# Performance work log

Measured on AMD Instinct MI355X. Metric: run time of the kernel, lower is better.

The kernel has to match this reference:

```python
import jax, jax.numpy as jnp
import numpy as np

B, T, S, D, H, F = 4, 1024, 1024, 1024, 16, 4096
NEG = jnp.float32(-1e9)


def _ln(x, g, b):
    m = jnp.mean(x, axis=-1, keepdims=True)
    v = jnp.mean((x - m) ** 2, axis=-1, keepdims=True)
    return (x - m) * jax.lax.rsqrt(v + 1e-5) * g + b


def _mha(q, k, v, wq, bq, wk, bk, wv, bv, wo, bo, scale, mask, causal, sbias):
    Bq, Tq, Dq = q.shape
    Sk = k.shape[1]
    dk = Dq // H
    Q = (q @ wq.T + bq).reshape(Bq, Tq, H, dk).transpose(0, 2, 1, 3)  # [B,H,T,dk]
    K = (k @ wk.T + bk).reshape(Bq, Sk, H, dk).transpose(0, 2, 1, 3)  # [B,H,S,dk]
    V = (v @ wv.T + bv).reshape(Bq, Sk, H, dk).transpose(0, 2, 1, 3)
    s = jnp.einsum('bhtd,bhsd->bhts', Q, K) / jnp.sqrt(jnp.float32(dk))
    if sbias is not None:
        s = s + scale * sbias[:, None, None, :]
    if mask is not None:
        s = jnp.where(mask == 0, NEG, s)
    if causal is not None:
        s = jnp.where(causal == 0, NEG, s)
    a = jax.nn.softmax(s, axis=-1)
    o = jnp.einsum('bhts,bhsd->bhtd', a, V).transpose(0, 2, 1, 3).reshape(Bq, Tq, Dq)
    return o @ wo.T + bo


def setup_inputs():
    key = jax.random.key(0)
    ks = jax.random.split(key, 16)
    r = lambda i, shape, s=0.02: jax.random.normal(ks[i], shape, dtype=jnp.float32) * s
    z = lambda *shape: jnp.zeros(shape, jnp.float32)
    o = lambda *shape: jnp.ones(shape, jnp.float32)
    inp = dict(
        x=r(0, (B, T, D), 1.0),
        memory=r(1, (B, S, D), 1.0),
        sentence_bias=r(2, (B, S), 1.0),
        trg_mask=jnp.ones((B, 1, 1, T), jnp.int32),
        trg_causal_mask=jnp.tril(jnp.ones((T, T), jnp.int32))[None, None],
        src_mask=jnp.ones((B, 1, 1, S), jnp.int32),
        sa_wq=r(3, (D, D)), sa_bq=z(D), sa_wk=r(4, (D, D)), sa_bk=z(D),
        sa_wv=r(5, (D, D)), sa_bv=z(D), sa_wo=r(6, (D, D)), sa_bo=z(D),
        sa_scale=jnp.float32(0.1),
        ca_wq=r(7, (D, D)), ca_bq=z(D), ca_wk=r(8, (D, D)), ca_bk=z(D),
        ca_wv=r(9, (D, D)), ca_bv=z(D), ca_wo=r(10, (D, D)), ca_bo=z(D),
        ca_scale=jnp.float32(0.1),
        ln1_g=o(D), ln1_b=z(D), ln2_g=o(D), ln2_b=z(D), ln3_g=o(D), ln3_b=z(D),
        ffn_w1=r(11, (F, D)), ffn_b1=z(F), ffn_w2=r(12, (D, F)), ffn_b2=z(D),
    )
    return inp


def reference(x, memory, trg_mask, trg_causal_mask, src_mask, sentence_bias,
              sa_wq, sa_bq, sa_wk, sa_bk, sa_wv, sa_bv, sa_wo, sa_bo, sa_scale,
              ca_wq, ca_bq, ca_wk, ca_bk, ca_wv, ca_bv, ca_wo, ca_bo, ca_scale,
              ln1_g, ln1_b, ln2_g, ln2_b, ln3_g, ln3_b,
              ffn_w1, ffn_b1, ffn_w2, ffn_b2):
    # Faithful quirk: Q comes from normed x, K/V from raw residual stream.
    x = x + _mha(_ln(x, ln1_g, ln1_b), x, x,
                 sa_wq, sa_bq, sa_wk, sa_bk, sa_wv, sa_bv, sa_wo, sa_bo,
                 sa_scale, trg_mask, trg_causal_mask, None)
    x = x + _mha(_ln(x, ln2_g, ln2_b), memory, memory,
                 ca_wq, ca_bq, ca_wk, ca_bk, ca_wv, ca_bv, ca_wo, ca_bo,
                 ca_scale, src_mask, None, sentence_bias)
    h = _ln(x, ln3_g, ln3_b)
    x = x + (jax.nn.relu(h @ ffn_w1.T + ffn_b1) @ ffn_w2.T + ffn_b2)
    return x
```

## Files before the change

### kernel.cpp

```cpp
#include <hip/hip_runtime.h>
#include <hip/hip_bf16.h>
#include <cmath>
#include <stdint.h>

typedef __hip_bfloat16 bf16;
typedef __attribute__((ext_vector_type(8))) __bf16 bf16x8;
typedef __attribute__((ext_vector_type(8))) unsigned short u16x8;
typedef __attribute__((ext_vector_type(4))) float f32x4;

__device__ __forceinline__ void gld16(const void* g, const void* l)
{
    __builtin_amdgcn_global_load_lds(
        (const __attribute__((address_space(1))) unsigned int*)(unsigned long long)g,
        (__attribute__((address_space(3))) unsigned int*)(unsigned int)(unsigned long long)l,
        16, 0, 0);
}

struct CvtSrcs { const float* p[24]; };

__global__ __launch_bounds__(256) void cvt_all(
    CvtSrcs s, bf16* __restrict__ dst,
    const float* __restrict__ lg, const float* __restrict__ lb,
    bf16* __restrict__ lnout)
{
    const int t = threadIdx.x;
    const int i = (blockIdx.x * 256 + t) * 8;
    const int seg = i >> 20;
    const float* sp = s.p[seg] + (i & 1048575);
    const float4 a = *(const float4*)(sp);
    const float4 b = *(const float4*)(sp + 4);
    const float v[8] = {a.x, a.y, a.z, a.w, b.x, b.y, b.z, b.w};
    bf16 tmp[8];
#pragma unroll
    for (int j = 0; j < 8; ++j) tmp[j] = __float2bfloat16(v[j]);
    *(uint4*)(dst + i) = *(const uint4*)tmp;

    if (seg < 4) {
        float s1 = 0.f, s2 = 0.f;
#pragma unroll
        for (int j = 0; j < 8; ++j) { s1 += v[j]; s2 += v[j] * v[j]; }
#pragma unroll
        for (int off = 32; off > 0; off >>= 1) {
            s1 += __shfl_xor(s1, off, 64);
            s2 += __shfl_xor(s2, off, 64);
        }
        __shared__ float r1[4], r2[4];
        const int w = t >> 6;
        if ((t & 63) == 0) { r1[w] = s1; r2[w] = s2; }
        __syncthreads();
        const int rw = (w >> 1) * 2;
        s1 = r1[rw] + r1[rw + 1];
        s2 = r2[rw] + r2[rw + 1];
        const float mean = s1 * (1.f / 1024.f);
        const float var  = s2 * (1.f / 1024.f) - mean * mean;
        const float rstd = rsqrtf(var + 1e-5f);
        bf16 lt[8];
        const int c0 = i & 1023;
#pragma unroll
        for (int j = 0; j < 8; ++j)
            lt[j] = __float2bfloat16((v[j] - mean) * rstd * lg[c0 + j] + lb[c0 + j]);
        *(uint4*)(lnout + i) = *(const uint4*)lt;
    }
}

enum {
    EPI_QSCALE = 0,
    EPI_KV = 1,
    EPI_RELU = 2,
    EPI_RES_F32_F32OUT = 3,
    EPI_PART = 4
};

template <int EPI>
__device__ __forceinline__ void body64(
    unsigned short* __restrict__ sAp, unsigned short* __restrict__ sBp,
    const bf16* __restrict__ A, const bf16* __restrict__ W,
    const float* __restrict__ bias, const float* __restrict__ bias2,
    const float* __restrict__ res, void* __restrict__ out,
    int N, int Kiter, int Kstride, int bx)
{
    const int t  = threadIdx.x;
    const int l  = t & 63;
    const int w  = t >> 6;
    const int wv = w * 64;
    const int wr = w >> 1;
    const int wc = w & 1;
    const int lm = l & 15;
    const int kq = l >> 4;
    const int rx = lm & 7;

    const int xcd = bx & 7;
    const int ib  = bx >> 3;
    const int bm  = xcd * 4 + (ib & 3);
    const int bn  = ib >> 2;

    const bf16* gA = A + (size_t)(bm * 128 + (t >> 3)) * Kstride
                       + ((t & 7) ^ ((t >> 3) & 7)) * 8;
    const bf16* gB = W + (size_t)(bn * 64 + (t >> 3)) * Kstride
                       + ((t & 7) ^ ((t >> 3) & 7)) * 8;

#define SQA_B(slot, kt, j)                                      \
    gld16(gA + (size_t)((j) * 32) * Kstride + (kt) * 64,        \
          sAp + (slot) * 8192 + ((j) * 256 + wv) * 8)
#define SQB_B(slot, kt, j)                                      \
    gld16(gB + (size_t)((j) * 32) * Kstride + (kt) * 64,        \
          sBp + (slot) * 4096 + ((j) * 256 + wv) * 8)

    bf16x8 af[4][2], bg[2][2];

#define READ_A_B(s_, mh, kk)                                                \
    do {                                                                    \
        _Pragma("unroll")                                                   \
        for (int m2 = 0; m2 < 2; ++m2) {                                    \
            const int mi = (mh) * 2 + m2;                                   \
            const int lr = wr * 64 + mi * 16 + lm;                          \
            const int sl = (((kk) << 2) | kq) ^ rx;                         \
            af[mi][kk] = __builtin_bit_cast(bf16x8,                         \
                *(const u16x8*)(sAp + (s_) * 8192 + lr * 64 + sl * 8));     \
        }                                                                   \
    } while (0)
#define READ_B_B(s_, kk)                                                    \
    do {                                                                    \
        _Pragma("unroll")                                                   \
        for (int ni = 0; ni < 2; ++ni) {                                    \
            const int lr = wc * 32 + ni * 16 + lm;                          \
            const int sl = (((kk) << 2) | kq) ^ rx;                         \
            bg[ni][kk] = __builtin_bit_cast(bf16x8,                         \
                *(const u16x8*)(sBp + (s_) * 4096 + lr * 64 + sl * 8));     \
        }                                                                   \
    } while (0)
#define MFMA_PH_B(mh, kk)                                                   \
    do {                                                                    \
        __builtin_amdgcn_s_setprio(1);                                      \
        _Pragma("unroll")                                                   \
        for (int m2 = 0; m2 < 2; ++m2)                                      \
            _Pragma("unroll")                                               \
            for (int ni = 0; ni < 2; ++ni)                                  \
                acc[(mh) * 2 + m2][ni] =                                    \
                    __builtin_amdgcn_mfma_f32_16x16x32_bf16(                \
                        af[(mh) * 2 + m2][kk], bg[ni][kk],                  \
                        acc[(mh) * 2 + m2][ni], 0, 0, 0);                   \
        __builtin_amdgcn_s_setprio(0);                                      \
    } while (0)
#define BARRIER_B() do { __builtin_amdgcn_s_barrier();                      \
                         __builtin_amdgcn_sched_barrier(0); } while (0)
#define WAITV0_B() asm volatile("s_waitcnt vmcnt(0)" ::: "memory")

    f32x4 acc[4][2] = {};
    const int NT = Kiter >> 6;

    SQB_B(0, 0, 0); SQB_B(0, 0, 1);
    SQA_B(0, 0, 0); SQA_B(0, 0, 1); SQA_B(0, 0, 2); SQA_B(0, 0, 3);

    for (int tt = 0; tt < NT; ++tt) {
        const int s = tt & 1, d = s ^ 1, kn = tt + 1;
        WAITV0_B(); BARRIER_B();
        if (kn < NT) {
            SQB_B(d, kn, 0); SQB_B(d, kn, 1);
            SQA_B(d, kn, 0); SQA_B(d, kn, 1); SQA_B(d, kn, 2); SQA_B(d, kn, 3);
        }
        READ_A_B(s, 0, 0); READ_B_B(s, 0);
        MFMA_PH_B(0, 0);
        READ_A_B(s, 1, 0);
        MFMA_PH_B(1, 0);
        READ_A_B(s, 1, 1); READ_B_B(s, 1);
        MFMA_PH_B(1, 1);
        READ_A_B(s, 0, 1);
        MFMA_PH_B(0, 1);
    }
#undef SQA_B
#undef SQB_B
#undef READ_A_B
#undef READ_B_B
#undef MFMA_PH_B
#undef BARRIER_B
#undef WAITV0_B

#pragma unroll
    for (int ni = 0; ni < 2; ++ni) {
        const int col = bn * 64 + wc * 32 + ni * 16 + lm;
        float bv = 0.f;
        if (EPI == EPI_KV) bv = (col < 1024) ? bias[col] : bias2[col - 1024];
        else bv = bias[col];
#pragma unroll
        for (int mi = 0; mi < 4; ++mi) {
#pragma unroll
            for (int r = 0; r < 4; ++r) {
                const int row = bm * 128 + wr * 64 + mi * 16 + kq * 4 + r;
                float v = acc[mi][ni][r] + bv;
                if (EPI == EPI_QSCALE) v *= 0.125f;
                if (EPI == EPI_KV) {
                    if (col < 1024) {
                        ((bf16*)out)[(size_t)row * 1024 + col] = __float2bfloat16(v);
                    } else {
                        const int ch = col - 1024;
                        const size_t idx = (size_t)4 * 1048576 +
                            ((size_t)((row >> 10) * 16 + (ch >> 6)) * 64 + (ch & 63)) * 1024
                            + (row & 1023);
                        ((bf16*)out)[idx] = __float2bfloat16(v);
                    }
                } else if (EPI == EPI_RES_F32_F32OUT) {
                    const size_t idx = (size_t)row * N + col;
                    ((float*)out)[idx] = v + res[idx];
                } else {
                    ((bf16*)out)[(size_t)row * N + col] = __float2bfloat16(v);
                }
            }
        }
    }
}

template <int EPI>
__global__ __launch_bounds__(256, 3) void gemm_n64(
    const bf16* __restrict__ A, const bf16* __restrict__ W,
    const float* __restrict__ bias, const float* __restrict__ bias2,
    const float* __restrict__ res, void* __restrict__ out,
    int M, int N, int Kiter, int Kstride)
{
    __shared__ __align__(16) unsigned short sA[2 * 128 * 64];
    __shared__ __align__(16) unsigned short sB[2 * 64 * 64];
    body64<EPI>(sA, sB, A, W, bias, bias2, res, out,
                N, Kiter, Kstride, blockIdx.x);
}

__global__ __launch_bounds__(256, 3) void qkv_fused(
    const bf16* __restrict__ Aq, const bf16* __restrict__ Wq,
    const float* __restrict__ bq, bf16* __restrict__ Qb,
    const bf16* __restrict__ Akv, const bf16* __restrict__ Wkv,
    const float* __restrict__ bk, const float* __restrict__ bv,
    bf16* __restrict__ Kb)
{
    __shared__ __align__(16) unsigned short sA[2 * 128 * 64];
    __shared__ __align__(16) unsigned short sB[2 * 64 * 64];
    const int bx = blockIdx.x;
    if (bx < 512)
        body64<EPI_QSCALE>(sA, sB, Aq, Wq, bq, nullptr, nullptr, Qb,
                           1024, 1024, 1024, bx);
    else
        body64<EPI_KV>(sA, sB, Akv, Wkv, bk, bv, nullptr, Kb,
                       2048, 1024, 1024, bx - 512);
}

template <int EPI>
__global__ __launch_bounds__(256, 2) void gemm_n128(
    const bf16* __restrict__ A, const bf16* __restrict__ W,
    const float* __restrict__ bias, void* __restrict__ out,
    int N, int Kiter, int Kstride)
{
    __shared__ __align__(16) unsigned short sAp[2 * 128 * 64];
    __shared__ __align__(16) unsigned short sBp[2 * 128 * 64];

    const int t  = threadIdx.x;
    const int l  = t & 63;
    const int w  = t >> 6;
    const int wv = w * 64;
    const int wr = w >> 1;
    const int wc = w & 1;
    const int lm = l & 15;
    const int kq = l >> 4;
    const int rx = lm & 7;

    const int bx  = blockIdx.x;
    const int xcd = bx & 7;
    const int ib  = bx >> 3;
    const int bm  = xcd * 4 + (ib & 3);
    const int bn  = ib >> 2;

    const bf16* gA = A + (size_t)(bm * 128 + (t >> 3)) * Kstride
                       + ((t & 7) ^ ((t >> 3) & 7)) * 8;
    const bf16* gB = W + (size_t)(bn * 128 + (t >> 3)) * Kstride
                       + ((t & 7) ^ ((t >> 3) & 7)) * 8;

#define SQA_C(slot, kt, j)                                      \
    gld16(gA + (size_t)((j) * 32) * Kstride + (kt) * 64,        \
          sAp + (slot) * 8192 + ((j) * 256 + wv) * 8)
#define SQB_C(slot, kt, j)                                      \
    gld16(gB + (size_t)((j) * 32) * Kstride + (kt) * 64,        \
          sBp + (slot) * 8192 + ((j) * 256 + wv) * 8)

    bf16x8 af[4], bg[4];

#define READ_A_C(s_, kk)                                                    \
    do {                                                                    \
        _Pragma("unroll")                                                   \
        for (int mi = 0; mi < 4; ++mi) {                                    \
            const int lr = wr * 64 + mi * 16 + lm;                          \
            const int sl = (((kk) << 2) | kq) ^ rx;                         \
            af[mi] = __builtin_bit_cast(bf16x8,                             \
                *(const u16x8*)(sAp + (s_) * 8192 + lr * 64 + sl * 8));     \
        }                                                                   \
    } while (0)
#define READ_B_C(s_, kk)                                                    \
    do {                                                                    \
        _Pragma("unroll")                                                   \
        for (int ni = 0; ni < 4; ++ni) {                                    \
            const int lr = wc * 64 + ni * 16 + lm;                          \
            const int sl = (((kk) << 2) | kq) ^ rx;                         \
            bg[ni] = __builtin_bit_cast(bf16x8,                             \
                *(const u16x8*)(sBp + (s_) * 8192 + lr * 64 + sl * 8));     \
        }                                                                   \
    } while (0)
#define MFMA_PH_C()                                                         \
    do {                                                                    \
        __builtin_amdgcn_s_setprio(1);                                      \
        _Pragma("unroll")                                                   \
        for (int mi = 0; mi < 4; ++mi)                                      \
            _Pragma("unroll")                                               \
            for (int ni = 0; ni < 4; ++ni)                                  \
                acc[mi][ni] = __builtin_amdgcn_mfma_f32_16x16x32_bf16(      \
                    af[mi], bg[ni], acc[mi][ni], 0, 0, 0);                  \
        __builtin_amdgcn_s_setprio(0);                                      \
    } while (0)
#define BARRIER_C() do { __builtin_amdgcn_s_barrier();                      \
                         __builtin_amdgcn_sched_barrier(0); } while (0)
#define WAITV0_C() asm volatile("s_waitcnt vmcnt(0)" ::: "memory")

    f32x4 acc[4][4] = {};
    const int NT = Kiter >> 6;

    SQB_C(0, 0, 0); SQB_C(0, 0, 1); SQB_C(0, 0, 2); SQB_C(0, 0, 3);
    SQA_C(0, 0, 0); SQA_C(0, 0, 1); SQA_C(0, 0, 2); SQA_C(0, 0, 3);

    for (int tt = 0; tt < NT; ++tt) {
        const int s = tt & 1, d = s ^ 1, kn = tt + 1;
        WAITV0_C(); BARRIER_C();
        if (kn < NT) {
            SQB_C(d, kn, 0); SQB_C(d, kn, 1); SQB_C(d, kn, 2); SQB_C(d, kn, 3);
            SQA_C(d, kn, 0); SQA_C(d, kn, 1); SQA_C(d, kn, 2); SQA_C(d, kn, 3);
        }
        READ_A_C(s, 0); READ_B_C(s, 0);
        MFMA_PH_C();
        READ_A_C(s, 1); READ_B_C(s, 1);
        MFMA_PH_C();
    }
#undef SQA_C
#undef SQB_C
#undef READ_A_C
#undef READ_B_C
#undef MFMA_PH_C
#undef BARRIER_C
#undef WAITV0_C

    __syncthreads();
    unsigned short* scr = sAp + w * 4096;
#pragma unroll
    for (int ni = 0; ni < 4; ++ni) {
        const int col = bn * 128 + wc * 64 + ni * 16 + lm;
        const float bv = bias[col];
        const int c  = ni * 2 + (lm >> 3);
        const int ci = lm & 7;
#pragma unroll
        for (int mi = 0; mi < 4; ++mi)
#pragma unroll
            for (int r = 0; r < 4; ++r) {
                const int row = mi * 16 + kq * 4 + r;
                float v = acc[mi][ni][r] + bv;
                if (EPI == EPI_RELU) v = fmaxf(v, 0.f);
                scr[row * 64 + ((c ^ (row & 7)) * 8) + ci] =
                    __builtin_bit_cast(unsigned short, (__bf16)v);
            }
    }
    asm volatile("s_waitcnt lgkmcnt(0)" ::: "memory");
#pragma unroll
    for (int it = 0; it < 8; ++it) {
        const int row = it * 8 + (l >> 3);
        const int lc  = l & 7;
        const u16x8 vv = *(const u16x8*)&scr[row * 64 + ((lc ^ (row & 7)) * 8)];
        const int Crow = bm * 128 + wr * 64 + row;
        const int Ccol = bn * 128 + wc * 64 + lc * 8;
        *(u16x8*)((bf16*)out + (size_t)Crow * N + Ccol) = vv;
    }
}

template <bool CAUSAL, bool SBIAS>
__global__ __launch_bounds__(256, 2) void flash_attn(
    const bf16* __restrict__ Q, const bf16* __restrict__ K,
    const bf16* __restrict__ Vt, bf16* __restrict__ O,
    const float* __restrict__ sbias, const float* __restrict__ scale_ptr)
{
    __shared__ __align__(16) unsigned short sK[2][64 * 64];
    __shared__ __align__(16) unsigned short sV[2][64 * 64];
    __shared__ __align__(16) unsigned short sP[4 * 32 * 72];

    const int t  = threadIdx.x;
    const int l  = t & 63;
    const int w  = t >> 6;
    const int wv = w * 64;
    const int lm = l & 15;
    const int kq = l >> 4;

    const int bh = blockIdx.x & 63;
    const int qb = blockIdx.x >> 6;
    const int h  = bh & 15;
    const int b  = bh >> 4;

    const int tb = qb * 128 + w * 32;
    const size_t qrow0 = (size_t)(b * 1024 + tb) * 1024 + h * 64;

    bf16x8 qf[2][2];
#pragma unroll
    for (int mi = 0; mi < 2; ++mi)
#pragma unroll
        for (int kk = 0; kk < 2; ++kk)
            qf[mi][kk] = __builtin_bit_cast(bf16x8,
                *(const u16x8*)(Q + qrow0 + (size_t)(mi * 16 + lm) * 1024 + kk * 32 + kq * 8));

    float cs = 0.f; const float* sb = nullptr;
    if (SBIAS) { cs = scale_ptr[0]; sb = sbias + b * 1024; }

    const bf16* gK = K  + (size_t)(b * 1024 + (t >> 3)) * 1024 + h * 64
                   + ((t & 7) ^ ((t >> 3) & 7)) * 8;
    const bf16* gV = Vt + (size_t)((b * 16 + h) * 64 + (t >> 3)) * 1024
                   + ((t & 7) ^ ((t >> 3) & 7)) * 8;
    __bf16* sPw = (__bf16*)sP + w * 32 * 72;

#define STAGE_KV(buf, s0r)                                                   \
    do {                                                                     \
        gld16(gK + (size_t)(s0r) * 1024,        &sK[buf][wv * 8]);           \
        gld16(gK + (size_t)((s0r) + 32) * 1024, &sK[buf][2048 + wv * 8]);    \
        gld16(gV + (s0r),                       &sV[buf][wv * 8]);           \
        gld16(gV + (s0r) + 32 * 1024,           &sV[buf][2048 + wv * 8]);    \
    } while (0)

    const int niter = CAUSAL ? (2 * qb + 2) : 16;

    STAGE_KV(0, 0);
    __syncthreads();

    f32x4 acc_o[2][4] = {};
    f32x4 l_run[2] = {};

    for (int it = 0; it < niter; ++it) {
        const int s0 = it * 64;
        const int cur = it & 1;

        if (it + 1 < niter) STAGE_KV(cur ^ 1, s0 + 64);

        f32x4 accs[2][4] = {};
#pragma unroll
        for (int ni = 0; ni < 4; ++ni)
#pragma unroll
            for (int kk = 0; kk < 2; ++kk) {
                const bf16x8 kf = __builtin_bit_cast(bf16x8,
                    *(const u16x8*)(&sK[cur][(ni * 16 + lm) * 64
                        + ((((kk << 2) | kq)) ^ (lm & 7)) * 8]));
#pragma unroll
                for (int mi = 0; mi < 2; ++mi)
                    accs[mi][ni] = __builtin_amdgcn_mfma_f32_16x16x32_bf16(
                        qf[mi][kk], kf, accs[mi][ni], 0, 0, 0);
            }

        if (SBIAS) {
#pragma unroll
            for (int ni = 0; ni < 4; ++ni) {
                const float sv = cs * sb[s0 + ni * 16 + lm];
#pragma unroll
                for (int mi = 0; mi < 2; ++mi)
#pragma unroll
                    for (int r = 0; r < 4; ++r) accs[mi][ni][r] += sv;
            }
        }
        if (CAUSAL && (s0 + 63 > tb)) {
#pragma unroll
            for (int ni = 0; ni < 4; ++ni) {
                const int s = s0 + ni * 16 + lm;
#pragma unroll
                for (int mi = 0; mi < 2; ++mi)
#pragma unroll
                    for (int r = 0; r < 4; ++r)
                        if (s > tb + mi * 16 + kq * 4 + r) accs[mi][ni][r] = -1e30f;
            }
        }

#pragma unroll
        for (int mi = 0; mi < 2; ++mi)
#pragma unroll
            for (int ni = 0; ni < 4; ++ni)
#pragma unroll
                for (int r = 0; r < 4; ++r) {
                    const float e = __expf(accs[mi][ni][r]);
                    l_run[mi][r] += e;
                    sPw[(mi * 16 + kq * 4 + r) * 72 + ni * 16 + lm] = (__bf16)e;
                }

#pragma unroll
        for (int kk = 0; kk < 2; ++kk) {
            bf16x8 pf[2];
#pragma unroll
            for (int mi = 0; mi < 2; ++mi)
                pf[mi] = __builtin_bit_cast(bf16x8,
                    *(const u16x8*)(sPw + (mi * 16 + lm) * 72 + kk * 32 + kq * 8));
#pragma unroll
            for (int di = 0; di < 4; ++di) {
                const bf16x8 vf = __builtin_bit_cast(bf16x8,
                    *(const u16x8*)(&sV[cur][(di * 16 + lm) * 64
                        + ((((kk << 2) | kq)) ^ (lm & 7)) * 8]));
#pragma unroll
                for (int mi = 0; mi < 2; ++mi)
                    acc_o[mi][di] = __builtin_amdgcn_mfma_f32_16x16x32_bf16(
                        pf[mi], vf, acc_o[mi][di], 0, 0, 0);
            }
        }

        __syncthreads();
    }
#undef STAGE_KV

#pragma unroll
    for (int mi = 0; mi < 2; ++mi) {
        f32x4 lt = l_run[mi];
#pragma unroll
        for (int x = 1; x < 16; x <<= 1)
#pragma unroll
            for (int r = 0; r < 4; ++r) lt[r] += __shfl_xor(lt[r], x, 64);
#pragma unroll
        for (int r = 0; r < 4; ++r) lt[r] = 1.f / lt[r];
#pragma unroll
        for (int di = 0; di < 4; ++di)
#pragma unroll
            for (int r = 0; r < 4; ++r) {
                const size_t idx = (size_t)(b * 1024 + tb + mi * 16 + kq * 4 + r) * 1024
                                 + h * 64 + di * 16 + lm;
                O[idx] = __float2bfloat16(acc_o[mi][di][r] * lt[r]);
            }
    }
}

__global__ __launch_bounds__(256) void ln_kernel(
    const float* __restrict__ xin, const float* __restrict__ g,
    const float* __restrict__ bta, bf16* __restrict__ out)
{
    const int row = blockIdx.x;
    const int t = threadIdx.x;
    const size_t base = (size_t)row * 1024 + t * 4;

    const float4 f = *(const float4*)(xin + base);
    const float v[4] = {f.x, f.y, f.z, f.w};
    float s1 = v[0] + v[1] + v[2] + v[3];
    float s2 = v[0]*v[0] + v[1]*v[1] + v[2]*v[2] + v[3]*v[3];
#pragma unroll
    for (int off = 32; off > 0; off >>= 1) {
        s1 += __shfl_xor(s1, off, 64);
        s2 += __shfl_xor(s2, off, 64);
    }
    __shared__ float r1[4], r2[4];
    if ((t & 63) == 0) { r1[t >> 6] = s1; r2[t >> 6] = s2; }
    __syncthreads();
    s1 = r1[0] + r1[1] + r1[2] + r1[3];
    s2 = r2[0] + r2[1] + r2[2] + r2[3];
    const float mean = s1 * (1.f / 1024.f);
    const float var  = s2 * (1.f / 1024.f) - mean * mean;
    const float rstd = rsqrtf(var + 1e-5f);
#pragma unroll
    for (int j = 0; j < 4; ++j) {
        const int c = t * 4 + j;
        out[base + j] = __float2bfloat16((v[j] - mean) * rstd * g[c] + bta[c]);
    }
}

extern "C" void kernel_launch(void* const* d_in, const int* in_sizes, int n_in,
                              void* d_out, int out_size, void* d_ws, size_t ws_size,
                              hipStream_t stream)
{
    const float* x       = (const float*)d_in[0];
    const float* memory  = (const float*)d_in[1];
    const float* sbias   = (const float*)d_in[2];
    const float* sa_bq = (const float*)d_in[7];
    const float* sa_bk = (const float*)d_in[9];
    const float* sa_bv = (const float*)d_in[11];
    const float* sa_bo = (const float*)d_in[13];
    const float* ca_bq = (const float*)d_in[16];
    const float* ca_bk = (const float*)d_in[18];
    const float* ca_bv = (const float*)d_in[20];
    const float* ca_bo = (const float*)d_in[22];
    const float* ca_scale = (const float*)d_in[23];
    const float* ln1_g = (const float*)d_in[24]; const float* ln1_b = (const float*)d_in[25];
    const float* ln2_g = (const float*)d_in[26]; const float* ln2_b = (const float*)d_in[27];
    const float* ln3_g = (const float*)d_in[28]; const float* ln3_b = (const float*)d_in[29];
    const float* b1 = (const float*)d_in[31];
    const float* b2 = (const float*)d_in[33];

    char* ws = (char*)d_ws;
    const size_t MB = (size_t)1 << 20;
    float* x1    = (float*)(ws + 0 * MB);
    float* x2    = (float*)(ws + 16 * MB);
    bf16* lnbuf  = (bf16*)(ws + 32 * MB);
    bf16* Qb     = (bf16*)(ws + 40 * MB);
    bf16* Kb     = (bf16*)(ws + 48 * MB);
    bf16* Vtb    = (bf16*)(ws + 56 * MB);
    bf16* Ob     = (bf16*)(ws + 64 * MB);
    bf16* ffnmid = (bf16*)(ws + 40 * MB);
    bf16* wx     = (bf16*)(ws + 72 * MB);
    bf16* wmem   = (bf16*)(ws + 80 * MB);
    bf16* bw     = (bf16*)(ws + 88 * MB);
    bf16* b_sa_wq = bw + 0 * 1048576, *b_sa_wk = bw + 1 * 1048576;
    bf16* b_sa_wo = bw + 3 * 1048576;
    bf16* b_ca_wq = bw + 4 * 1048576, *b_ca_wk = bw + 5 * 1048576;
    bf16* b_ca_wo = bw + 7 * 1048576;
    bf16* b_w1   = (bf16*)(ws + 104 * MB);
    bf16* b_w2   = (bf16*)(ws + 112 * MB);

    const int M = 4096;
    dim3 blk256(256);
    const dim3 gQ(512);
    const dim3 gQKV(1536);
    const dim3 gFA(512);
    const dim3 gF1(1024);

    CvtSrcs cs;
    for (int c = 0; c < 4; ++c) {
        cs.p[c]      = x + (size_t)c * 1048576;
        cs.p[4 + c]  = memory + (size_t)c * 1048576;
        cs.p[16 + c] = (const float*)d_in[30] + (size_t)c * 1048576;
        cs.p[20 + c] = (const float*)d_in[32] + (size_t)c * 1048576;
    }
    cs.p[8]  = (const float*)d_in[6];
    cs.p[9]  = (const float*)d_in[8];
    cs.p[10] = (const float*)d_in[10];
    cs.p[11] = (const float*)d_in[12];
    cs.p[12] = (const float*)d_in[15];
    cs.p[13] = (const float*)d_in[17];
    cs.p[14] = (const float*)d_in[19];
    cs.p[15] = (const float*)d_in[21];
    cvt_all<<<24 * 1048576 / 2048, blk256, 0, stream>>>(
        cs, wx, ln1_g, ln1_b, lnbuf);

    qkv_fused<<<gQKV, blk256, 0, stream>>>(
        lnbuf, b_sa_wq, sa_bq, Qb, wx, b_sa_wk, sa_bk, sa_bv, Kb);
    flash_attn<true, false><<<gFA, blk256, 0, stream>>>(Qb, Kb, Vtb, Ob, nullptr, nullptr);
    gemm_n64<EPI_RES_F32_F32OUT><<<gQ, blk256, 0, stream>>>(
        Ob, b_sa_wo, sa_bo, nullptr, x, x1, M, 1024, 1024, 1024);

    ln_kernel<<<4096, blk256, 0, stream>>>(x1, ln2_g, ln2_b, lnbuf);
    qkv_fused<<<gQKV, blk256, 0, stream>>>(
        lnbuf, b_ca_wq, ca_bq, Qb, wmem, b_ca_wk, ca_bk, ca_bv, Kb);
    flash_attn<false, true><<<gFA, blk256, 0, stream>>>(Qb, Kb, Vtb, Ob, sbias, ca_scale);
    gemm_n64<EPI_RES_F32_F32OUT><<<gQ, blk256, 0, stream>>>(
        Ob, b_ca_wo, ca_bo, nullptr, x1, x2, M, 1024, 1024, 1024);

    ln_kernel<<<4096, blk256, 0, stream>>>(x2, ln3_g, ln3_b, lnbuf);
    gemm_n128<EPI_RELU><<<gF1, blk256, 0, stream>>>(
        lnbuf, b_w1, b1, ffnmid, 4096, 1024, 1024);
    gemm_n64<EPI_RES_F32_F32OUT><<<gQ, blk256, 0, stream>>>(
        ffnmid, b_w2, b2, nullptr, x2, d_out, M, 1024, 4096, 4096);
}
```

Baseline: 460.9 us.

## Use a 64x64-tile GEMM kernel for the FFN down-projection

Adds a new 128-thread GEMM kernel with 64x64 output tiles and uses it for the FFN second matmul (M=4096, N=1024, K=4096), doubling the grid from 512 to 1024 blocks. The previous 128x64 tiling launched only 512 blocks for a long-K GEMM, which may underfill the GPU's compute units. The smaller tiles cost more redundant global and LDS traffic per FLOP and fewer MFMAs per barrier.

New measurement: 458.0 us. Within noise of the previous version (-0.6%).

```diff
diff --git a/kernel.cpp b/kernel.cpp
--- a/kernel.cpp
+++ b/kernel.cpp
@@ -241,6 +241,118 @@
                        2048, 1024, 1024, bx - 512);
 }
 
+__global__ __launch_bounds__(128, 3) void gemm_s64(
+    const bf16* __restrict__ A, const bf16* __restrict__ W,
+    const float* __restrict__ bias, const float* __restrict__ res,
+    float* __restrict__ out, int N, int Kiter, int Kstride)
+{
+    __shared__ __align__(16) unsigned short sA[2 * 64 * 64];
+    __shared__ __align__(16) unsigned short sB[2 * 64 * 64];
+
+    const int t  = threadIdx.x;
+    const int l  = t & 63;
+    const int w  = t >> 6;
+    const int wv = w * 64;
+    const int lm = l & 15;
+    const int kq = l >> 4;
+    const int rx = lm & 7;
+
+    const int bx  = blockIdx.x;
+    const int xcd = bx & 7;
+    const int ib  = bx >> 3;
+    const int bm  = xcd * 8 + (ib & 7);
+    const int bn  = ib >> 3;
+
+    const bf16* gA = A + (size_t)(bm * 64 + (t >> 3)) * Kstride
+                       + ((t & 7) ^ ((t >> 3) & 7)) * 8;
+    const bf16* gB = W + (size_t)(bn * 64 + (t >> 3)) * Kstride
+                       + ((t & 7) ^ ((t >> 3) & 7)) * 8;
+
+#define SQA_S(slot, kt, j)                                      \
+    gld16(gA + (size_t)((j) * 16) * Kstride + (kt) * 64,        \
+          sA + (slot) * 4096 + ((j) * 128 + wv) * 8)
+#define SQB_S(slot, kt, j)                                      \
+    gld16(gB + (size_t)((j) * 16) * Kstride + (kt) * 64,        \
+          sB + (slot) * 4096 + ((j) * 128 + wv) * 8)
+
+    bf16x8 af[4], bg[2];
+
+#define READ_A_S(s_, kk)                                                    \
+    do {                                                                    \
+        _Pragma("unroll")                                                   \
+        for (int mi = 0; mi < 4; ++mi) {                                    \
+            const int lr = mi * 16 + lm;                                    \
+            const int sl = (((kk) << 2) | kq) ^ rx;                         \
+            af[mi] = __builtin_bit_cast(bf16x8,                             \
+                *(const u16x8*)(sA + (s_) * 4096 + lr * 64 + sl * 8));      \
+        }                                                                   \
+    } while (0)
+#define READ_B_S(s_, kk)                                                    \
+    do {                                                                    \
+        _Pragma("unroll")                                                   \
+        for (int ni = 0; ni < 2; ++ni) {                                    \
+            const int lr = w * 32 + ni * 16 + lm;                           \
+            const int sl = (((kk) << 2) | kq) ^ rx;                         \
+            bg[ni] = __builtin_bit_cast(bf16x8,                             \
+                *(const u16x8*)(sB + (s_) * 4096 + lr * 64 + sl * 8));      \
+        }                                                                   \
+    } while (0)
+#define MFMA_PH_S()                                                         \
+    do {                                                                    \
+        __builtin_amdgcn_s_setprio(1);                                      \
+        _Pragma("unroll")                                                   \
+        for (int mi = 0; mi < 4; ++mi)                                      \
+            _Pragma("unroll")                                               \
+            for (int ni = 0; ni < 2; ++ni)                                  \
+                acc[mi][ni] = __builtin_amdgcn_mfma_f32_16x16x32_bf16(      \
+                    af[mi], bg[ni], acc[mi][ni], 0, 0, 0);                  \
+        __builtin_amdgcn_s_setprio(0);                                      \
+    } while (0)
+#define BARRIER_S() do { __builtin_amdgcn_s_barrier();                      \
+                         __builtin_amdgcn_sched_barrier(0); } while (0)
+#define WAITV0_S() asm volatile("s_waitcnt vmcnt(0)" ::: "memory")
+
+    f32x4 acc[4][2] = {};
+    const int NT = Kiter >> 6;
+
+    SQB_S(0, 0, 0); SQB_S(0, 0, 1); SQB_S(0, 0, 2); SQB_S(0, 0, 3);
+    SQA_S(0, 0, 0); SQA_S(0, 0, 1); SQA_S(0, 0, 2); SQA_S(0, 0, 3);
+
+    for (int tt = 0; tt < NT; ++tt) {
+        const int s = tt & 1, d = s ^ 1, kn = tt + 1;
+        WAITV0_S(); BARRIER_S();
+        if (kn < NT) {
+            SQB_S(d, kn, 0); SQB_S(d, kn, 1); SQB_S(d, kn, 2); SQB_S(d, kn, 3);
+            SQA_S(d, kn, 0); SQA_S(d, kn, 1); SQA_S(d, kn, 2); SQA_S(d, kn, 3);
+        }
+        READ_A_S(s, 0); READ_B_S(s, 0);
+        MFMA_PH_S();
+        READ_A_S(s, 1); READ_B_S(s, 1);
+        MFMA_PH_S();
+    }
+#undef SQA_S
+#undef SQB_S
+#undef READ_A_S
+#undef READ_B_S
+#undef MFMA_PH_S
+#undef BARRIER_S
+#undef WAITV0_S
+
+#pragma unroll
+    for (int ni = 0; ni < 2; ++ni) {
+        const int col = bn * 64 + w * 32 + ni * 16 + lm;
+        const float bv = bias[col];
+#pragma unroll
+        for (int mi = 0; mi < 4; ++mi)
+#pragma unroll
+            for (int r = 0; r < 4; ++r) {
+                const int row = bm * 64 + mi * 16 + kq * 4 + r;
+                const size_t idx = (size_t)row * N + col;
+                out[idx] = acc[mi][ni][r] + bv + res[idx];
+            }
+    }
+}
+
 template <int EPI>
 __global__ __launch_bounds__(256, 2) void gemm_n128(
     const bf16* __restrict__ A, const bf16* __restrict__ W,
@@ -601,11 +713,12 @@
     bf16* b_w2   = (bf16*)(ws + 112 * MB);
 
     const int M = 4096;
-    dim3 blk256(256);
+    dim3 blk256(256), blk128(128);
     const dim3 gQ(512);
     const dim3 gQKV(1536);
     const dim3 gFA(512);
     const dim3 gF1(1024);
+    const dim3 gF2(1024);
 
     CvtSrcs cs;
     for (int c = 0; c < 4; ++c) {
@@ -641,6 +754,6 @@
     ln_kernel<<<4096, blk256, 0, stream>>>(x2, ln3_g, ln3_b, lnbuf);
     gemm_n128<EPI_RELU><<<gF1, blk256, 0, stream>>>(
         lnbuf, b_w1, b1, ffnmid, 4096, 1024, 1024);
-    gemm_n64<EPI_RES_F32_F32OUT><<<gQ, blk256, 0, stream>>>(
-        ffnmid, b_w2, b2, nullptr, x2, d_out, M, 1024, 4096, 4096);
-}
+    gemm_s64<<<gF2, blk128, 0, stream>>>(
+        ffnmid, b_w2, b2, x2, (float*)d_out, 1024, 4096, 4096);
+}
```
